# Optimization experiments

Hardware: AMD Instinct MI355X
Metric: run time of the kernel (lower is better)

The kernel has to match this reference:

```python
import jax, jax.numpy as jnp
import numpy as np
import math

B, L, D = 2, 2048, 1024
H = 16
DH = D // H  # 64
XPOS_SCALE_BASE = 512.0
THETA = 10000.0


def setup_inputs() -> dict:
    key = jax.random.key(0)
    ks = jax.random.split(key, 9)
    s = 0.02  # keep logits in a sane range like trained weights
    return {
        "x": jax.random.normal(ks[0], (B, L, D), dtype=jnp.float32),
        "Wq": jax.random.normal(ks[1], (D, D), dtype=jnp.float32) * s,
        "bq": jax.random.normal(ks[2], (D,), dtype=jnp.float32) * s,
        "Wk": jax.random.normal(ks[3], (D, D), dtype=jnp.float32) * s,
        "bk": jax.random.normal(ks[4], (D,), dtype=jnp.float32) * s,
        "Wv": jax.random.normal(ks[5], (D, D), dtype=jnp.float32) * s,
        "bv": jax.random.normal(ks[6], (D,), dtype=jnp.float32) * s,
        "Wo": jax.random.normal(ks[7], (D, D), dtype=jnp.float32) * s,
        "bo": jax.random.normal(ks[8], (D,), dtype=jnp.float32) * s,
    }


def _rotate_half(t):
    # pairwise interleaved rotation, as in rotary_embedding_torch
    t1 = t[..., 0::2]
    t2 = t[..., 1::2]
    return jnp.stack([-t2, t1], axis=-1).reshape(t.shape)


def _xpos_rotate(q, k):
    # q, k: [B, H, L, DH]; xPos rotary embedding (use_xpos=True)
    seq = q.shape[2]
    half = jnp.arange(0, DH, 2, dtype=jnp.float32)
    inv_freq = 1.0 / (THETA ** (half / DH))            # [DH/2]
    t = jnp.arange(seq, dtype=jnp.float32)             # [L]
    freqs = t[:, None] * inv_freq[None, :]             # [L, DH/2]
    freqs = jnp.repeat(freqs, 2, axis=-1)              # [L, DH] interleaved
    # xPos length-extrapolatable scale
    scale_vec = (half + 0.4 * DH) / (1.4 * DH)         # [DH/2]
    power = (t - seq // 2) / XPOS_SCALE_BASE           # [L]
    scale = scale_vec[None, :] ** power[:, None]       # [L, DH/2]
    scale = jnp.repeat(scale, 2, axis=-1)              # [L, DH]
    cos = jnp.cos(freqs)
    sin = jnp.sin(freqs)
    q_out = q * (cos * scale) + _rotate_half(q) * (sin * scale)
    k_out = k * (cos / scale) + _rotate_half(k) * (sin / scale)
    return q_out, k_out


def reference(x, Wq, bq, Wk, bk, Wv, bv, Wo, bo):
    b, l, d = x.shape
    # projections; note source swaps names: v_mat <- k-proj, k_mat <- v-proj
    q = (x @ Wq.T + bq).reshape(b, l, H, DH).transpose(0, 2, 1, 3)  # [b,h,l,dh]
    v = (x @ Wk.T + bk).reshape(b, l, H, DH).transpose(0, 2, 1, 3)
    k = (x @ Wv.T + bv).reshape(b, l, H, DH).transpose(0, 2, 1, 3)
    q, k = _xpos_rotate(q, k)
    # source divides by sqrt(Dh * num_heads) == sqrt(dim)
    scores = jnp.einsum("bhqd,bhkd->bhqk", q, k) / math.sqrt(d)
    weights = jax.nn.softmax(scores, axis=-1)
    inter = jnp.einsum("bhqk,bhkd->bhqd", weights, v)
    inter = inter.transpose(0, 2, 1, 3).reshape(b, l, d)
    return inter @ Wo.T + bo
```

## Files before the change

### kernel.cpp

```cpp
#include <hip/hip_runtime.h>
#include <math.h>

#define NB 2
#define NL 2048
#define ND 1024
#define NH 16
#define NDH 64
#define NBL 4096

typedef __attribute__((ext_vector_type(4))) float f32x4;
typedef __attribute__((ext_vector_type(8))) short s16x8;

__device__ __forceinline__ unsigned short f2bf(float f){
  unsigned int u = __float_as_uint(f);
  u += 0x7FFF + ((u >> 16) & 1);
  return (unsigned short)(u >> 16);
}

__device__ __forceinline__ unsigned int pk2bf(float lo, float hi){
  return __builtin_amdgcn_perm(__float_as_uint(hi) + 0x8000u,
                               __float_as_uint(lo) + 0x8000u, 0x07060302u);
}

__global__ void cvt_all(const float* __restrict__ x,
                        const float* __restrict__ wq, const float* __restrict__ wk,
                        const float* __restrict__ wv, const float* __restrict__ wo,
                        unsigned short* __restrict__ xb,
                        unsigned short* __restrict__ wqb, unsigned short* __restrict__ wkb,
                        unsigned short* __restrict__ wvb, unsigned short* __restrict__ wob){
  int i = blockIdx.x * blockDim.x + threadIdx.x;
  const float* s; unsigned short* d; int off;
  if (i < (1<<20)) { s = x; d = xb; off = i; }
  else {
    int j = i - (1<<20); int w = j >> 18; off = j & ((1<<18)-1);
    s = (w==0)?wq:(w==1)?wk:(w==2)?wv:wo;
    d = (w==0)?wqb:(w==1)?wkb:(w==2)?wvb:wob;
  }
  float4 f = reinterpret_cast<const float4*>(s)[off];
  ushort4 r; r.x=f2bf(f.x); r.y=f2bf(f.y); r.z=f2bf(f.z); r.w=f2bf(f.w);
  reinterpret_cast<ushort4*>(d)[off] = r;
}

__global__ void rope_tables(float* __restrict__ cosT, float* __restrict__ sinT, float* __restrict__ scT){
  int t = blockIdx.x * blockDim.x + threadIdx.x;
  int l = t >> 5, i = t & 31;
  float half = 2.0f * (float)i;
  float inv_freq = 1.0f / powf(10000.0f, half / 64.0f);
  float fr = (float)l * inv_freq;
  float sv = (half + 0.4f * 64.0f) / (1.4f * 64.0f);
  float pw = ((float)l - 1024.0f) / 512.0f;
  cosT[t] = cosf(fr);
  sinT[t] = sinf(fr);
  scT[t]  = powf(sv, pw);
}

__device__ __forceinline__ void gemm_core128(
    const unsigned short* __restrict__ A, const unsigned short* __restrict__ W,
    int row0, int col0,
    unsigned short (&As)[128][32], unsigned short (&Bs)[128][32],
    f32x4 (&acc)[4][4])
{
  const int tid  = threadIdx.x;
  const int wave = tid >> 6, lane = tid & 63;
  const int m16  = lane & 15, quad = lane >> 4;
  const int mrow = (wave & 1) * 64, ncol = (wave >> 1) * 64;
  const int rA   = lane >> 2, cA = (lane & 3) * 8;

  for (int k0 = 0; k0 < ND; k0 += 32){
    __syncthreads();
#pragma unroll
    for (int i2 = 0; i2 < 2; i2++){
      const int c = wave * 2 + i2;
      const unsigned short* ga = A + (size_t)(row0 + c*16 + rA) * ND + k0 + cA;
      const unsigned short* gb = W + (size_t)(col0 + c*16 + rA) * ND + k0 + cA;
      __builtin_amdgcn_global_load_lds((const __attribute__((address_space(1))) void*)ga,
                                       (__attribute__((address_space(3))) void*)&As[c*16][0], 16, 0, 0);
      __builtin_amdgcn_global_load_lds((const __attribute__((address_space(1))) void*)gb,
                                       (__attribute__((address_space(3))) void*)&Bs[c*16][0], 16, 0, 0);
    }
    __syncthreads();
    s16x8 af[4], bf[4];
#pragma unroll
    for (int mt = 0; mt < 4; mt++) af[mt] = *reinterpret_cast<const s16x8*>(&As[mrow + mt*16 + m16][quad*8]);
#pragma unroll
    for (int nt = 0; nt < 4; nt++) bf[nt] = *reinterpret_cast<const s16x8*>(&Bs[ncol + nt*16 + m16][quad*8]);
#pragma unroll
    for (int mt = 0; mt < 4; mt++)
#pragma unroll
      for (int nt = 0; nt < 4; nt++)
        acc[mt][nt] = __builtin_amdgcn_mfma_f32_16x16x32_bf16(af[mt], bf[nt], acc[mt][nt], 0, 0, 0);
  }
}

__global__ __launch_bounds__(256) void gemm_qkv(
    const unsigned short* __restrict__ A,
    const unsigned short* __restrict__ Wq, const float* __restrict__ bq,
    const unsigned short* __restrict__ Wk, const float* __restrict__ bk,
    const unsigned short* __restrict__ Wv, const float* __restrict__ bv,
    unsigned short* __restrict__ qb, unsigned short* __restrict__ kb,
    unsigned short* __restrict__ vtb,
    const float* __restrict__ cosT, const float* __restrict__ sinT, const float* __restrict__ scT)
{
  __shared__ unsigned short As[128][32];
  __shared__ unsigned short Bs[128][32];
  __shared__ unsigned short T[128][72];

  const int mode = blockIdx.z;
  const unsigned short* W = (mode==0) ? Wq : (mode==1) ? Wk : Wv;
  const float* bias       = (mode==0) ? bq : (mode==1) ? bk : bv;

  const int row0 = blockIdx.x * 128, col0 = blockIdx.y * 128;
  f32x4 acc[4][4] = {};
  gemm_core128(A, W, row0, col0, As, Bs, acc);

  const int tid  = threadIdx.x;
  const int wave = tid >> 6, lane = tid & 63;
  const int m16  = lane & 15, quad = lane >> 4;
  const int mrow = (wave & 1) * 64, ncol = (wave >> 1) * 64;

  if (mode == 2){
    const int b = row0 >> 11, l0 = row0 & (NL - 1);
#pragma unroll
    for (int h2 = 0; h2 < 2; h2++){
      __syncthreads();
      if ((wave >> 1) == h2){
#pragma unroll
        for (int mt = 0; mt < 4; mt++)
#pragma unroll
          for (int nt = 0; nt < 4; nt++)
#pragma unroll
            for (int r = 0; r < 4; r++){
              int lrow = mrow + mt*16 + quad*4 + r;
              int dh   = nt*16 + m16;
              T[lrow][dh] = f2bf(acc[mt][nt][r] + bias[col0 + h2*64 + dh]);
            }
      }
      __syncthreads();
      const int bh = b * NH + (col0 >> 6) + h2;
#pragma unroll
      for (int j4 = 0; j4 < 4; j4++){
        int c = tid * 4 + j4;
        int d = c >> 4, seg = (c & 15) * 8;
        unsigned short tmp[8];
#pragma unroll
        for (int jj = 0; jj < 8; jj++) tmp[jj] = T[seg + jj][d];
        *reinterpret_cast<uint4*>(vtb + (size_t)(bh * NDH + d) * NL + l0 + seg) =
            *reinterpret_cast<uint4*>(tmp);
      }
    }
  } else {
    const float qscale = (mode == 0) ? 0.03125f : 1.0f;
    unsigned short* dst = (mode == 0) ? qb : kb;
#pragma unroll
    for (int mt = 0; mt < 4; mt++)
#pragma unroll
      for (int nt = 0; nt < 4; nt++)
#pragma unroll
        for (int r = 0; r < 4; r++){
          int grow = row0 + mrow + mt*16 + quad*4 + r;
          int gcol = col0 + ncol + nt*16 + m16;
          float v = acc[mt][nt][r] + bias[gcol];
          int b = grow >> 11, l = grow & (NL - 1);
          int h = gcol >> 6, dh = gcol & 63;
          float pv = __shfl_xor(v, 1);
          int ti = l*32 + (dh >> 1);
          float cs = cosT[ti], sn = sinT[ti], sc = scT[ti];
          if (mode == 1) sc = 1.0f / sc;
          float rh = (dh & 1) ? pv : -pv;
          float ov = (v * cs + rh * sn) * sc * qscale;
          dst[(((size_t)(b * NH + h)) * NL + l) * NDH + dh] = f2bf(ov);
        }
  }
}

__global__ __launch_bounds__(256) void gemm_o(
    const unsigned short* __restrict__ A, const unsigned short* __restrict__ W,
    const float* __restrict__ bias, float* __restrict__ out)
{
  __shared__ unsigned short As[128][32];
  __shared__ unsigned short Bs[64][32];
  const int tid  = threadIdx.x;
  const int wave = tid >> 6, lane = tid & 63;
  const int m16  = lane & 15, quad = lane >> 4;
  const int mrow = (wave & 1) * 64, ncol = (wave >> 1) * 32;
  const int rA   = lane >> 2, cA = (lane & 3) * 8;
  const int row0 = blockIdx.x * 128, col0 = blockIdx.y * 64;

  f32x4 acc[4][2] = {};

  for (int k0 = 0; k0 < ND; k0 += 32){
    __syncthreads();
#pragma unroll
    for (int i3 = 0; i3 < 3; i3++){
      const int c = wave * 3 + i3;
      const unsigned short* g; unsigned short* l;
      if (c < 8){ g = A + (size_t)(row0 + c*16 + rA) * ND + k0 + cA;      l = &As[c*16][0]; }
      else      { g = W + (size_t)(col0 + (c-8)*16 + rA) * ND + k0 + cA;  l = &Bs[(c-8)*16][0]; }
      __builtin_amdgcn_global_load_lds((const __attribute__((address_space(1))) void*)g,
                                       (__attribute__((address_space(3))) void*)l, 16, 0, 0);
    }
    __syncthreads();
    s16x8 af[4], bf[2];
#pragma unroll
    for (int mt = 0; mt < 4; mt++) af[mt] = *reinterpret_cast<const s16x8*>(&As[mrow + mt*16 + m16][quad*8]);
#pragma unroll
    for (int nt = 0; nt < 2; nt++) bf[nt] = *reinterpret_cast<const s16x8*>(&Bs[ncol + nt*16 + m16][quad*8]);
#pragma unroll
    for (int mt = 0; mt < 4; mt++)
#pragma unroll
      for (int nt = 0; nt < 2; nt++)
        acc[mt][nt] = __builtin_amdgcn_mfma_f32_16x16x32_bf16(af[mt], bf[nt], acc[mt][nt], 0, 0, 0);
  }

#pragma unroll
  for (int mt = 0; mt < 4; mt++)
#pragma unroll
    for (int nt = 0; nt < 2; nt++)
#pragma unroll
      for (int r = 0; r < 4; r++){
        int grow = row0 + mrow + mt*16 + quad*4 + r;
        int gcol = col0 + ncol + nt*16 + m16;
        out[(size_t)grow * ND + gcol] = acc[mt][nt][r] + bias[gcol];
      }
}

__global__ __launch_bounds__(256, 2) void attn_kernel(
    const unsigned short* __restrict__ qb,
    const unsigned short* __restrict__ kb,
    const unsigned short* __restrict__ vtb,
    unsigned short* __restrict__ ob)
{
  __shared__ unsigned short Ks[64][72];
  __shared__ unsigned short Vs[64][72];
  __shared__ unsigned short Ps[128][72];

  const int tid  = threadIdx.x;
  const int wave = tid >> 6, lane = tid & 63;
  const int m16  = lane & 15, quad = lane >> 4;
  const int bh   = blockIdx.y;
  const int q0   = blockIdx.x * 128;
  const unsigned short* Q  = qb  + (size_t)bh * NL * NDH;
  const unsigned short* K  = kb  + (size_t)bh * NL * NDH;
  const unsigned short* Vt = vtb + (size_t)bh * NDH * NL;

  s16x8 qf[2][2];
#pragma unroll
  for (int qt = 0; qt < 2; qt++)
#pragma unroll
    for (int ks = 0; ks < 2; ks++)
      qf[qt][ks] = *reinterpret_cast<const s16x8*>(
          Q + (size_t)(q0 + wave*32 + qt*16 + m16) * NDH + ks*32 + quad*8);

  float ls[2] = {0.f, 0.f};
  f32x4 ot[4][2] = {};

  for (int kt = 0; kt < 32; kt++){
    __syncthreads();
    const int k0 = kt * 64;
#pragma unroll
    for (int it = 0; it < 2; it++){
      int idx = tid + it*256;
      int r = idx >> 3, sg = (idx & 7) * 8;
      *reinterpret_cast<uint4*>(&Ks[r][sg]) =
          *reinterpret_cast<const uint4*>(K + (size_t)(k0 + r) * NDH + sg);
      *reinterpret_cast<uint4*>(&Vs[r][sg]) =
          *reinterpret_cast<const uint4*>(Vt + (size_t)r * NL + k0 + sg);
    }
    __syncthreads();

    s16x8 kf[4][2], vf[4][2];
#pragma unroll
    for (int mt = 0; mt < 4; mt++)
#pragma unroll
      for (int ks = 0; ks < 2; ks++){
        kf[mt][ks] = *reinterpret_cast<const s16x8*>(&Ks[mt*16 + m16][ks*32 + quad*8]);
        vf[mt][ks] = *reinterpret_cast<const s16x8*>(&Vs[mt*16 + m16][ks*32 + quad*8]);
      }

    f32x4 st[2][4] = {};
#pragma unroll
    for (int qt = 0; qt < 2; qt++)
#pragma unroll
      for (int mt = 0; mt < 4; mt++)
#pragma unroll
        for (int ks = 0; ks < 2; ks++)
          st[qt][mt] = __builtin_amdgcn_mfma_f32_16x16x32_bf16(kf[mt][ks], qf[qt][ks], st[qt][mt], 0, 0, 0);

#pragma unroll
    for (int qt = 0; qt < 2; qt++){
#pragma unroll
      for (int mt = 0; mt < 4; mt++){
        float e0 = __expf(st[qt][mt][0]);
        float e1 = __expf(st[qt][mt][1]);
        float e2 = __expf(st[qt][mt][2]);
        float e3 = __expf(st[qt][mt][3]);
        ls[qt] += (e0 + e1) + (e2 + e3);
        uint2 pk; pk.x = pk2bf(e0, e1); pk.y = pk2bf(e2, e3);
        *reinterpret_cast<uint2*>(&Ps[wave*32 + qt*16 + m16][mt*16 + quad*4]) = pk;
      }
    }

    s16x8 pf[2][2];
#pragma unroll
    for (int qt = 0; qt < 2; qt++)
#pragma unroll
      for (int ks = 0; ks < 2; ks++)
        pf[qt][ks] = *reinterpret_cast<const s16x8*>(&Ps[wave*32 + qt*16 + m16][ks*32 + quad*8]);
#pragma unroll
    for (int mt = 0; mt < 4; mt++)
#pragma unroll
      for (int qt = 0; qt < 2; qt++)
#pragma unroll
        for (int ks = 0; ks < 2; ks++)
          ot[mt][qt] = __builtin_amdgcn_mfma_f32_16x16x32_bf16(vf[mt][ks], pf[qt][ks], ot[mt][qt], 0, 0, 0);
  }

  float linv[2];
#pragma unroll
  for (int qt = 0; qt < 2; qt++){
    float t = ls[qt];
    t += __shfl_xor(t, 16);
    t += __shfl_xor(t, 32);
    linv[qt] = 1.0f / t;
  }

#pragma unroll
  for (int mt = 0; mt < 4; mt++)
#pragma unroll
    for (int qt = 0; qt < 2; qt++){
      float o0 = ot[mt][qt][0] * linv[qt];
      float o1 = ot[mt][qt][1] * linv[qt];
      float o2 = ot[mt][qt][2] * linv[qt];
      float o3 = ot[mt][qt][3] * linv[qt];
      uint2 pk; pk.x = pk2bf(o0, o1); pk.y = pk2bf(o2, o3);
      *reinterpret_cast<uint2*>(&Ps[wave*32 + qt*16 + m16][mt*16 + quad*4]) = pk;
    }
  __syncthreads();

  const int bb = bh >> 4, h = bh & 15;
  const int row = tid >> 1, half = tid & 1;
  unsigned short* dst = ob + ((size_t)(bb*NL + q0 + row)) * ND + h*NDH + half*32;
#pragma unroll
  for (int j = 0; j < 4; j++)
    *reinterpret_cast<uint4*>(dst + j*8) = *reinterpret_cast<const uint4*>(&Ps[row][half*32 + j*8]);
}

extern "C" void kernel_launch(void* const* d_in, const int* in_sizes, int n_in,
                              void* d_out, int out_size, void* d_ws, size_t ws_size,
                              hipStream_t stream)
{
  (void)in_sizes; (void)n_in; (void)out_size; (void)ws_size;
  const float* x  = (const float*)d_in[0];
  const float* Wq = (const float*)d_in[1];
  const float* bq = (const float*)d_in[2];
  const float* Wk = (const float*)d_in[3];
  const float* bk = (const float*)d_in[4];
  const float* Wv = (const float*)d_in[5];
  const float* bv = (const float*)d_in[6];
  const float* Wo = (const float*)d_in[7];
  const float* bo = (const float*)d_in[8];
  float* out = (float*)d_out;

  char* p = (char*)d_ws;
  unsigned short* xb   = (unsigned short*)p; p += (size_t)NBL*ND*2;
  unsigned short* wqb  = (unsigned short*)p; p += (size_t)ND*ND*2;
  unsigned short* wkb  = (unsigned short*)p; p += (size_t)ND*ND*2;
  unsigned short* wvb  = (unsigned short*)p; p += (size_t)ND*ND*2;
  unsigned short* wob  = (unsigned short*)p; p += (size_t)ND*ND*2;
  unsigned short* qbuf = (unsigned short*)p; p += (size_t)NBL*ND*2;
  unsigned short* kbuf = (unsigned short*)p; p += (size_t)NBL*ND*2;
  unsigned short* vtb  = (unsigned short*)p; p += (size_t)NBL*ND*2;
  unsigned short* ibuf = (unsigned short*)p; p += (size_t)NBL*ND*2;
  float* cosT = (float*)p; p += (size_t)NL*32*4;
  float* sinT = (float*)p; p += (size_t)NL*32*4;
  float* scT  = (float*)p; p += (size_t)NL*32*4;

  hipLaunchKernelGGL(cvt_all, dim3(8192), dim3(256), 0, stream,
                     x, Wq, Wk, Wv, Wo, xb, wqb, wkb, wvb, wob);
  hipLaunchKernelGGL(rope_tables, dim3(NL*32/256), dim3(256), 0, stream, cosT, sinT, scT);

  hipLaunchKernelGGL(gemm_qkv, dim3(NBL/128, ND/128, 3), dim3(256), 0, stream,
                     xb, wqb, bq, wvb, bv, wkb, bk, qbuf, kbuf, vtb, cosT, sinT, scT);

  hipLaunchKernelGGL(attn_kernel, dim3(NL/128, NB*NH), dim3(256), 0, stream,
                     qbuf, kbuf, vtb, ibuf);

  hipLaunchKernelGGL(gemm_o, dim3(NBL/128, ND/64), dim3(256), 0, stream, ibuf, wob, bo, out);
}
```

Measured before the change: 224.4 us.

## Rewrite attention with 32x32 MFMA, register-held P, swizzled LDS and prefetch

The attention kernel moves from 16x16x32 to 32x32 MFMA tiles. The exponentiated scores stay in registers and feed the PV MFMA directly instead of round-tripping through shared memory. K/V tiles go into XOR-swizzled LDS without padding, and the next tile is prefetched into registers during compute. Softmax uses exp2 with log2e folded into the Q scale, and the rope tables are premultiplied by the xPos scale into float2 q/k tables. The risks are higher register pressure and the correctness of the P-to-B-operand layout mapping.

```diff
diff --git a/kernel.cpp b/kernel.cpp
--- a/kernel.cpp
+++ b/kernel.cpp
@@ -8,8 +8,20 @@
 #define NDH 64
 #define NBL 4096
 
-typedef __attribute__((ext_vector_type(4))) float f32x4;
-typedef __attribute__((ext_vector_type(8))) short s16x8;
+typedef __attribute__((ext_vector_type(4)))  float f32x4;
+typedef __attribute__((ext_vector_type(16))) float f32x16;
+typedef __attribute__((ext_vector_type(8)))  short s16x8;
+typedef __attribute__((ext_vector_type(4)))  short s16x4;
+
+#define LOG2E 1.44269504088896f
+
+__device__ __forceinline__ float fexp2(float x){
+#if __has_builtin(__builtin_amdgcn_exp2f)
+  return __builtin_amdgcn_exp2f(x);
+#else
+  return exp2f(x);
+#endif
+}
 
 __device__ __forceinline__ unsigned short f2bf(float f){
   unsigned int u = __float_as_uint(f);
@@ -41,7 +53,7 @@
   reinterpret_cast<ushort4*>(d)[off] = r;
 }
 
-__global__ void rope_tables(float* __restrict__ cosT, float* __restrict__ sinT, float* __restrict__ scT){
+__global__ void rope_tables(float2* __restrict__ qtab, float2* __restrict__ ktab){
   int t = blockIdx.x * blockDim.x + threadIdx.x;
   int l = t >> 5, i = t & 31;
   float half = 2.0f * (float)i;
@@ -49,9 +61,10 @@
   float fr = (float)l * inv_freq;
   float sv = (half + 0.4f * 64.0f) / (1.4f * 64.0f);
   float pw = ((float)l - 1024.0f) / 512.0f;
-  cosT[t] = cosf(fr);
-  sinT[t] = sinf(fr);
-  scT[t]  = powf(sv, pw);
+  float sc = powf(sv, pw);
+  float cs = cosf(fr), sn = sinf(fr);
+  qtab[t] = make_float2(cs * sc, sn * sc);
+  ktab[t] = make_float2(cs / sc, sn / sc);
 }
 
 __device__ __forceinline__ void gemm_core128(
@@ -99,7 +112,7 @@
     const unsigned short* __restrict__ Wv, const float* __restrict__ bv,
     unsigned short* __restrict__ qb, unsigned short* __restrict__ kb,
     unsigned short* __restrict__ vtb,
-    const float* __restrict__ cosT, const float* __restrict__ sinT, const float* __restrict__ scT)
+    const float2* __restrict__ qtab, const float2* __restrict__ ktab)
 {
   __shared__ unsigned short As[128][32];
   __shared__ unsigned short Bs[128][32];
@@ -149,7 +162,8 @@
       }
     }
   } else {
-    const float qscale = (mode == 0) ? 0.03125f : 1.0f;
+    const float qscale = (mode == 0) ? (0.03125f * LOG2E) : 1.0f;
+    const float2* tab  = (mode == 0) ? qtab : ktab;
     unsigned short* dst = (mode == 0) ? qb : kb;
 #pragma unroll
     for (int mt = 0; mt < 4; mt++)
@@ -163,11 +177,9 @@
           int b = grow >> 11, l = grow & (NL - 1);
           int h = gcol >> 6, dh = gcol & 63;
           float pv = __shfl_xor(v, 1);
-          int ti = l*32 + (dh >> 1);
-          float cs = cosT[ti], sn = sinT[ti], sc = scT[ti];
-          if (mode == 1) sc = 1.0f / sc;
+          float2 t = tab[l*32 + (dh >> 1)];
           float rh = (dh & 1) ? pv : -pv;
-          float ov = (v * cs + rh * sn) * sc * qscale;
+          float ov = (v * t.x + rh * t.y) * qscale;
           dst[(((size_t)(b * NH + h)) * NL + l) * NDH + dh] = f2bf(ov);
         }
   }
@@ -230,119 +242,119 @@
     const unsigned short* __restrict__ vtb,
     unsigned short* __restrict__ ob)
 {
-  __shared__ unsigned short Ks[64][72];
-  __shared__ unsigned short Vs[64][72];
-  __shared__ unsigned short Ps[128][72];
+  __shared__ unsigned short Ks[64 * 64];
+  __shared__ unsigned short Vs[64 * 64];
+  __shared__ unsigned short Os[128 * 72];
 
   const int tid  = threadIdx.x;
   const int wave = tid >> 6, lane = tid & 63;
-  const int m16  = lane & 15, quad = lane >> 4;
+  const int l31  = lane & 31, g = lane >> 5;
   const int bh   = blockIdx.y;
   const int q0   = blockIdx.x * 128;
   const unsigned short* Q  = qb  + (size_t)bh * NL * NDH;
   const unsigned short* K  = kb  + (size_t)bh * NL * NDH;
   const unsigned short* Vt = vtb + (size_t)bh * NDH * NL;
 
-  s16x8 qf[2][2];
-#pragma unroll
-  for (int qt = 0; qt < 2; qt++)
-#pragma unroll
-    for (int ks = 0; ks < 2; ks++)
-      qf[qt][ks] = *reinterpret_cast<const s16x8*>(
-          Q + (size_t)(q0 + wave*32 + qt*16 + m16) * NDH + ks*32 + quad*8);
-
-  float ls[2] = {0.f, 0.f};
-  f32x4 ot[4][2] = {};
+  s16x8 qf[4];
+#pragma unroll
+  for (int s = 0; s < 4; s++)
+    qf[s] = *reinterpret_cast<const s16x8*>(
+        Q + (size_t)(q0 + wave*32 + l31) * NDH + s*16 + g*8);
+
+  const int r0 = tid >> 3,          c0 = tid & 7;
+  const int r1 = (tid + 256) >> 3,  c1 = tid & 7;
+  unsigned short* ksw0 = &Ks[r0*64 + ((c0 ^ (r0 & 7)) * 8)];
+  unsigned short* ksw1 = &Ks[r1*64 + ((c1 ^ (r1 & 7)) * 8)];
+  unsigned short* vsw0 = &Vs[r0*64 + ((c0 ^ (r0 & 7)) * 8)];
+  unsigned short* vsw1 = &Vs[r1*64 + ((c1 ^ (r1 & 7)) * 8)];
+
+  uint4 kreg0 = *reinterpret_cast<const uint4*>(K  + (size_t)r0 * NDH + c0*8);
+  uint4 kreg1 = *reinterpret_cast<const uint4*>(K  + (size_t)r1 * NDH + c1*8);
+  uint4 vreg0 = *reinterpret_cast<const uint4*>(Vt + (size_t)r0 * NL  + c0*8);
+  uint4 vreg1 = *reinterpret_cast<const uint4*>(Vt + (size_t)r1 * NL  + c1*8);
+
+  float ls = 0.f;
+  f32x16 ot[2] = {};
 
   for (int kt = 0; kt < 32; kt++){
     __syncthreads();
-    const int k0 = kt * 64;
-#pragma unroll
-    for (int it = 0; it < 2; it++){
-      int idx = tid + it*256;
-      int r = idx >> 3, sg = (idx & 7) * 8;
-      *reinterpret_cast<uint4*>(&Ks[r][sg]) =
-          *reinterpret_cast<const uint4*>(K + (size_t)(k0 + r) * NDH + sg);
-      *reinterpret_cast<uint4*>(&Vs[r][sg]) =
-          *reinterpret_cast<const uint4*>(Vt + (size_t)r * NL + k0 + sg);
-    }
-    __syncthreads();
-
-    s16x8 kf[4][2], vf[4][2];
-#pragma unroll
-    for (int mt = 0; mt < 4; mt++)
-#pragma unroll
-      for (int ks = 0; ks < 2; ks++){
-        kf[mt][ks] = *reinterpret_cast<const s16x8*>(&Ks[mt*16 + m16][ks*32 + quad*8]);
-        vf[mt][ks] = *reinterpret_cast<const s16x8*>(&Vs[mt*16 + m16][ks*32 + quad*8]);
-      }
-
-    f32x4 st[2][4] = {};
-#pragma unroll
-    for (int qt = 0; qt < 2; qt++)
-#pragma unroll
-      for (int mt = 0; mt < 4; mt++)
-#pragma unroll
-        for (int ks = 0; ks < 2; ks++)
-          st[qt][mt] = __builtin_amdgcn_mfma_f32_16x16x32_bf16(kf[mt][ks], qf[qt][ks], st[qt][mt], 0, 0, 0);
-
-#pragma unroll
-    for (int qt = 0; qt < 2; qt++){
-#pragma unroll
-      for (int mt = 0; mt < 4; mt++){
-        float e0 = __expf(st[qt][mt][0]);
-        float e1 = __expf(st[qt][mt][1]);
-        float e2 = __expf(st[qt][mt][2]);
-        float e3 = __expf(st[qt][mt][3]);
-        ls[qt] += (e0 + e1) + (e2 + e3);
-        uint2 pk; pk.x = pk2bf(e0, e1); pk.y = pk2bf(e2, e3);
-        *reinterpret_cast<uint2*>(&Ps[wave*32 + qt*16 + m16][mt*16 + quad*4]) = pk;
-      }
-    }
-
-    s16x8 pf[2][2];
-#pragma unroll
-    for (int qt = 0; qt < 2; qt++)
-#pragma unroll
-      for (int ks = 0; ks < 2; ks++)
-        pf[qt][ks] = *reinterpret_cast<const s16x8*>(&Ps[wave*32 + qt*16 + m16][ks*32 + quad*8]);
-#pragma unroll
-    for (int mt = 0; mt < 4; mt++)
-#pragma unroll
-      for (int qt = 0; qt < 2; qt++)
-#pragma unroll
-        for (int ks = 0; ks < 2; ks++)
-          ot[mt][qt] = __builtin_amdgcn_mfma_f32_16x16x32_bf16(vf[mt][ks], pf[qt][ks], ot[mt][qt], 0, 0, 0);
-  }
-
-  float linv[2];
-#pragma unroll
-  for (int qt = 0; qt < 2; qt++){
-    float t = ls[qt];
-    t += __shfl_xor(t, 16);
-    t += __shfl_xor(t, 32);
-    linv[qt] = 1.0f / t;
-  }
-
-#pragma unroll
-  for (int mt = 0; mt < 4; mt++)
-#pragma unroll
-    for (int qt = 0; qt < 2; qt++){
-      float o0 = ot[mt][qt][0] * linv[qt];
-      float o1 = ot[mt][qt][1] * linv[qt];
-      float o2 = ot[mt][qt][2] * linv[qt];
-      float o3 = ot[mt][qt][3] * linv[qt];
+    *reinterpret_cast<uint4*>(ksw0) = kreg0;
+    *reinterpret_cast<uint4*>(ksw1) = kreg1;
+    *reinterpret_cast<uint4*>(vsw0) = vreg0;
+    *reinterpret_cast<uint4*>(vsw1) = vreg1;
+    __syncthreads();
+
+    if (kt < 31){
+      const int k0n = (kt + 1) * 64;
+      kreg0 = *reinterpret_cast<const uint4*>(K  + (size_t)(k0n + r0) * NDH + c0*8);
+      kreg1 = *reinterpret_cast<const uint4*>(K  + (size_t)(k0n + r1) * NDH + c1*8);
+      vreg0 = *reinterpret_cast<const uint4*>(Vt + (size_t)r0 * NL + k0n + c0*8);
+      vreg1 = *reinterpret_cast<const uint4*>(Vt + (size_t)r1 * NL + k0n + c1*8);
+    }
+
+    f32x16 st[2] = {};
+#pragma unroll
+    for (int t = 0; t < 2; t++){
+      const int key = t*32 + l31;
+#pragma unroll
+      for (int s = 0; s < 4; s++){
+        const int cg = (2*s + g) ^ (key & 7);
+        s16x8 kf = *reinterpret_cast<const s16x8*>(&Ks[key*64 + cg*8]);
+        st[t] = __builtin_amdgcn_mfma_f32_32x32x16_bf16(kf, qf[s], st[t], 0, 0, 0);
+      }
+    }
+
+    unsigned int pe[2][8];
+#pragma unroll
+    for (int t = 0; t < 2; t++){
+#pragma unroll
+      for (int i = 0; i < 8; i++){
+        float e0 = fexp2(st[t][2*i]);
+        float e1 = fexp2(st[t][2*i + 1]);
+        ls += e0 + e1;
+        pe[t][i] = pk2bf(e0, e1);
+      }
+    }
+
+#pragma unroll
+    for (int mt = 0; mt < 2; mt++){
+      const int dh = mt*32 + l31;
+#pragma unroll
+      for (int s = 0; s < 8; s++){
+        const int cg = (s ^ (dh & 7));
+        s16x4 vf = *reinterpret_cast<const s16x4*>(&Vs[dh*64 + cg*8 + g*4]);
+        uint2 pb; pb.x = pe[s>>2][2*(s&3)]; pb.y = pe[s>>2][2*(s&3)+1];
+        s16x4 pf = *reinterpret_cast<const s16x4*>(&pb);
+        ot[mt] = __builtin_amdgcn_mfma_f32_32x32x8bf16_1k(vf, pf, ot[mt], 0, 0, 0);
+      }
+    }
+  }
+
+  float lt = ls + __shfl_xor(ls, 32);
+  float linv = 1.0f / lt;
+
+#pragma unroll
+  for (int mt = 0; mt < 2; mt++){
+#pragma unroll
+    for (int s = 0; s < 4; s++){
+      float o0 = ot[mt][4*s    ] * linv;
+      float o1 = ot[mt][4*s + 1] * linv;
+      float o2 = ot[mt][4*s + 2] * linv;
+      float o3 = ot[mt][4*s + 3] * linv;
       uint2 pk; pk.x = pk2bf(o0, o1); pk.y = pk2bf(o2, o3);
-      *reinterpret_cast<uint2*>(&Ps[wave*32 + qt*16 + m16][mt*16 + quad*4]) = pk;
-    }
+      *reinterpret_cast<uint2*>(&Os[(wave*32 + l31)*72 + mt*32 + s*8 + g*4]) = pk;
+    }
+  }
   __syncthreads();
 
   const int bb = bh >> 4, h = bh & 15;
-  const int row = tid >> 1, half = tid & 1;
-  unsigned short* dst = ob + ((size_t)(bb*NL + q0 + row)) * ND + h*NDH + half*32;
-#pragma unroll
-  for (int j = 0; j < 4; j++)
-    *reinterpret_cast<uint4*>(dst + j*8) = *reinterpret_cast<const uint4*>(&Ps[row][half*32 + j*8]);
+#pragma unroll
+  for (int j = 0; j < 4; j++){
+    int idx = tid * 4 + j;
+    int row = idx >> 3, cg = (idx & 7) * 8;
+    *reinterpret_cast<uint4*>(ob + ((size_t)(bb*NL + q0 + row)) * ND + h*NDH + cg) =
+        *reinterpret_cast<const uint4*>(&Os[row*72 + cg]);
+  }
 }
 
 extern "C" void kernel_launch(void* const* d_in, const int* in_sizes, int n_in,
@@ -371,16 +383,15 @@
   unsigned short* kbuf = (unsigned short*)p; p += (size_t)NBL*ND*2;
   unsigned short* vtb  = (unsigned short*)p; p += (size_t)NBL*ND*2;
   unsigned short* ibuf = (unsigned short*)p; p += (size_t)NBL*ND*2;
-  float* cosT = (float*)p; p += (size_t)NL*32*4;
-  float* sinT = (float*)p; p += (size_t)NL*32*4;
-  float* scT  = (float*)p; p += (size_t)NL*32*4;
+  float2* qtab = (float2*)p; p += (size_t)NL*32*8;
+  float2* ktab = (float2*)p; p += (size_t)NL*32*8;
 
   hipLaunchKernelGGL(cvt_all, dim3(8192), dim3(256), 0, stream,
                      x, Wq, Wk, Wv, Wo, xb, wqb, wkb, wvb, wob);
-  hipLaunchKernelGGL(rope_tables, dim3(NL*32/256), dim3(256), 0, stream, cosT, sinT, scT);
+  hipLaunchKernelGGL(rope_tables, dim3(NL*32/256), dim3(256), 0, stream, qtab, ktab);
 
   hipLaunchKernelGGL(gemm_qkv, dim3(NBL/128, ND/128, 3), dim3(256), 0, stream,
-                     xb, wqb, bq, wvb, bv, wkb, bk, qbuf, kbuf, vtb, cosT, sinT, scT);
+                     xb, wqb, bq, wvb, bv, wkb, bk, qbuf, kbuf, vtb, qtab, ktab);
 
   hipLaunchKernelGGL(attn_kernel, dim3(NL/128, NB*NH), dim3(256), 0, stream,
                      qbuf, kbuf, vtb, ibuf);
```

Measured after the change: 209.3 us. 1.07x faster.
